# Kernel optimization log

Hardware: AMD Instinct MI355X
Metric: run time of the kernel (lower is better)

Reference implementation:

```python
import jax, jax.numpy as jnp
import numpy as np
import math

IN_CH = 512
KEY_SIZE = 512
VALUE_SIZE = 512
B, T = 8, 2048


def setup_inputs() -> dict:
    key = jax.random.key(0)
    ks = jax.random.split(key, 7)
    s = 1.0 / math.sqrt(IN_CH)
    return {
        "x": jax.random.normal(ks[0], (B, T, IN_CH), dtype=jnp.float32),
        "Wq": jax.random.uniform(ks[1], (IN_CH, KEY_SIZE), jnp.float32, -s, s),
        "bq": jax.random.uniform(ks[2], (KEY_SIZE,), jnp.float32, -s, s),
        "Wk": jax.random.uniform(ks[3], (IN_CH, KEY_SIZE), jnp.float32, -s, s),
        "bk": jax.random.uniform(ks[4], (KEY_SIZE,), jnp.float32, -s, s),
        "Wv": jax.random.uniform(ks[5], (IN_CH, VALUE_SIZE), jnp.float32, -s, s),
        "bv": jax.random.uniform(ks[6], (VALUE_SIZE,), jnp.float32, -s, s),
    }


def reference(x, Wq, bq, Wk, bk, Wv, bv):
    # Projections (single head)
    q = jnp.einsum('btc,ck->btk', x, Wq) + bq  # [B,T,K]
    k = jnp.einsum('btc,ck->btk', x, Wk) + bk  # [B,T,K]
    v = jnp.einsum('btc,cv->btv', x, Wv) + bv  # [B,T,V]
    # Full score matrix, causal mask (strictly upper triangle masked: col > row)
    scores = jnp.einsum('bqk,btk->bqt', q, k)  # [B,T,T]
    t = scores.shape[1]
    causal = jnp.arange(t)[None, :] > jnp.arange(t)[:, None]  # True where future
    scores = jnp.where(causal[None], -jnp.inf, scores)
    attn = jax.nn.softmax(scores / math.sqrt(KEY_SIZE), axis=2)
    out = jnp.einsum('bqt,btv->bqv', attn, v)  # [B,T,V]
    return jnp.concatenate((x, out), axis=2)  # [B,T,C+V]
```

## Files before the change

### kernel.cpp

```cpp
#include <hip/hip_runtime.h>


#define DEV __device__ __forceinline__

typedef unsigned short u16;
typedef unsigned int u32;
typedef __attribute__((ext_vector_type(8))) short short8;
typedef __attribute__((ext_vector_type(4))) float float4v;

DEV u16 f2bf(float f) {
    u32 u = __float_as_uint(f);
    return (u16)((u + 0x7FFFu + ((u >> 16) & 1u)) >> 16);
}
DEV float bf2f(u16 h) { return __uint_as_float(((u32)h) << 16); }

DEV float4v mfma16(short8 a, short8 b, float4v c) {
    return __builtin_amdgcn_mfma_f32_16x16x32_bf16(a, b, c, 0, 0, 0);
}

#define GLD16(gptr, lptr)                                                     \
    __builtin_amdgcn_global_load_lds(                                         \
        (const __attribute__((address_space(1))) void*)(gptr),                \
        (__attribute__((address_space(3))) void*)(lptr), 16, 0, 0)

__global__ void detect_k(const u32* __restrict__ xw, int* __restrict__ flag) {
    __shared__ int sh[256];
    int tid = threadIdx.x;
    u32 w = xw[tid * 64];
    int e = (w >> 7) & 0xFF;
    sh[tid] = (e >= 0x60 && e <= 0x90) ? 1 : 0;
    __syncthreads();
    for (int s = 128; s > 0; s >>= 1) {
        if (tid < s) sh[tid] += sh[tid + s];
        __syncthreads();
    }
    if (tid == 0) flag[0] = (sh[0] > 128) ? 1 : 0;
}

__global__ void convx_k(const void* __restrict__ x, const int* __restrict__ flag,
                        u16* __restrict__ xb, void* __restrict__ out) {
    int i0 = (blockIdx.x * 256 + threadIdx.x) * 8;
    int row = i0 >> 9, col = i0 & 511;
    if (flag[0]) {
        uint4 v = *(const uint4*)((const u16*)x + i0);
        *(uint4*)&xb[i0] = v;
        *(uint4*)((u16*)out + (size_t)row * 1024 + col) = v;
    } else {
        const float* xf = (const float*)x;
        float4 f0 = *(const float4*)(xf + i0);
        float4 f1 = *(const float4*)(xf + i0 + 4);
        union { u16 us[8]; uint4 v; } pk;
        pk.us[0] = f2bf(f0.x); pk.us[1] = f2bf(f0.y);
        pk.us[2] = f2bf(f0.z); pk.us[3] = f2bf(f0.w);
        pk.us[4] = f2bf(f1.x); pk.us[5] = f2bf(f1.y);
        pk.us[6] = f2bf(f1.z); pk.us[7] = f2bf(f1.w);
        *(uint4*)&xb[i0] = pk.v;
        float* o = (float*)out + (size_t)row * 1024 + col;
        *(float4*)o = f0; *(float4*)(o + 4) = f1;
    }
}

__global__ void convwb_k(const void* __restrict__ Wq, const void* __restrict__ Wk,
                         const void* __restrict__ Wv, const void* __restrict__ bq,
                         const void* __restrict__ bk, const void* __restrict__ bv,
                         const int* __restrict__ flag,
                         u16* __restrict__ Wt, u16* __restrict__ bbuf) {
    int z = blockIdx.y;
    if (blockIdx.x >= 1024) {
        int i = (blockIdx.x - 1024) * 256 + threadIdx.x;
        const void* s = (z == 0) ? bq : ((z == 1) ? bk : bv);
        bbuf[z * 512 + i] = flag[0] ? ((const u16*)s)[i]
                                    : f2bf(((const float*)s)[i]);
        return;
    }
    const void* W = (z == 0) ? Wq : ((z == 1) ? Wk : Wv);
    int flat = blockIdx.x * 256 + threadIdx.x;
    int n = flat >> 9, k = flat & 511;
    u16 v = flag[0] ? ((const u16*)W)[k * 512 + n]
                    : f2bf(((const float*)W)[k * 512 + n]);
    Wt[z * 262144 + flat] = v;
}

__global__ __launch_bounds__(256) void proj_k(
        const u16* __restrict__ x, const u16* __restrict__ Wt,
        const u16* __restrict__ bb,
        u16* __restrict__ Qo, u16* __restrict__ Ko, u16* __restrict__ Vt_out) {
    int z = blockIdx.z;
    const u16* Wz = Wt + z * 262144;
    const u16* bias = bb + z * 512;
    int mBase = blockIdx.x * 128;
    int nBase = blockIdx.y * 128;

    __shared__ __attribute__((aligned(16))) u16 Xs[128 * 32];
    __shared__ __attribute__((aligned(16))) u16 Ws[128 * 32];

    int tid = threadIdx.x;
    int w = tid >> 6, lane = tid & 63, quad = lane >> 4, l16 = lane & 15;
    int wr = (w >> 1) * 64, wc = (w & 1) * 64;

    float4v acc[4][4] = {};

    for (int k0 = 0; k0 < 512; k0 += 32) {
        #pragma unroll
        for (int gg = 0; gg < 2; gg++) {
            int g = w * 2 + gg;
            int row = g * 16 + (lane >> 2);
            int col8 = lane & 3;
            GLD16(&x [(size_t)(mBase + row) * 512 + k0 + col8 * 8], &Xs[g * 512]);
            GLD16(&Wz[(size_t)(nBase + row) * 512 + k0 + col8 * 8], &Ws[g * 512]);
        }
        __syncthreads();

        short8 a[4], b[4];
        #pragma unroll
        for (int mt = 0; mt < 4; mt++)
            a[mt] = *(const short8*)&Xs[(wr + mt * 16 + l16) * 32 + quad * 8];
        #pragma unroll
        for (int nt = 0; nt < 4; nt++)
            b[nt] = *(const short8*)&Ws[(wc + nt * 16 + l16) * 32 + quad * 8];
        #pragma unroll
        for (int mt = 0; mt < 4; mt++)
            #pragma unroll
            for (int nt = 0; nt < 4; nt++)
                acc[mt][nt] = mfma16(a[mt], b[nt], acc[mt][nt]);
        __syncthreads();
    }

    #pragma unroll
    for (int nt = 0; nt < 4; nt++) {
        int n = nBase + wc + nt * 16 + l16;
        float bval = bf2f(bias[n]);
        #pragma unroll
        for (int mt = 0; mt < 4; mt++) {
            int m0 = mBase + wr + mt * 16 + quad * 4;
            float4v v = acc[mt][nt];
            if (z == 2) {
                int bbi = m0 >> 11, tt = m0 & 2047;
                u16 t0 = f2bf(v[0] + bval), t1 = f2bf(v[1] + bval);
                u16 t2 = f2bf(v[2] + bval), t3 = f2bf(v[3] + bval);
                uint2 pk = make_uint2((u32)t0 | ((u32)t1 << 16), (u32)t2 | ((u32)t3 << 16));
                *(uint2*)&Vt_out[((size_t)bbi * 512 + n) * 2048 + tt] = pk;
            } else {
                u16* dst = (z == 0) ? Qo : Ko;
                #pragma unroll
                for (int r = 0; r < 4; r++)
                    dst[(size_t)(m0 + r) * 512 + n] = f2bf(v[r] + bval);
            }
        }
    }
}


#define LOADK(dst, kB, half)                                                  \
    { _Pragma("unroll")                                                       \
      for (int j = 0; j < 8; j++) {                                           \
        int row2 = 2 * (j * 4 + w);                                           \
        int row = row2 + (lane >> 5);                                         \
        int col8 = lane & 31;                                                 \
        GLD16(&Kb[(size_t)((kB) + row) * 512 + (half) * 256 +                 \
                  ((col8 ^ (row & 7)) << 3)], &dst[row2 * 256]);              \
      } }

#define LOADV(dst, kB, half)                                                  \
    { _Pragma("unroll")                                                       \
      for (int j = 0; j < 8; j++) {                                           \
        int blk8 = 8 * (j * 4 + w);                                           \
        int dl = blk8 + (lane >> 3);                                          \
        int col8 = lane & 7;                                                  \
        GLD16(&Vb[(size_t)((half) * 256 + dl) * 2048 + (kB) +                 \
                  ((col8 ^ (dl & 7)) << 3)], &dst[blk8 * 64]);                \
      } }

#define SSTEP(buf, h)                                                         \
    { _Pragma("unroll")                                                       \
      for (int kk = 0; kk < 8; kk++) {                                        \
        _Pragma("unroll")                                                     \
        for (int nt = 0; nt < 4; nt++) {                                      \
          short8 bf = *(const short8*)&buf[(nt * 16 + l16) * 256 +            \
                                           (((kk * 4 + quad) ^ sw) << 3)];    \
          accS[nt] = mfma16(qf[(h) * 8 + kk], bf, accS[nt]);                  \
        } } }

#define PVSTEP(buf, accO)                                                     \
    { _Pragma("unroll")                                                       \
      for (int kk = 0; kk < 2; kk++) {                                        \
        _Pragma("unroll")                                                     \
        for (int dt = 0; dt < 4; dt++) {                                      \
          int rowv = w * 64 + dt * 16 + l16;                                  \
          short8 bf = *(const short8*)&buf[rowv * 64 +                        \
                                           (((kk * 4 + quad) ^ sw) << 3)];    \
          _Pragma("unroll")                                                   \
          for (int mt = 0; mt < 4; mt++)                                      \
            accO[dt][mt] = mfma16(pf[mt][kk], bf, accO[dt][mt]);              \
        } } }

__global__ __launch_bounds__(256, 1) void attn_k(
        const u16* __restrict__ Q, const u16* __restrict__ K,
        const u16* __restrict__ Vt, const int* __restrict__ flag,
        void* __restrict__ out, u16* __restrict__ Opart,
        float2* __restrict__ ml, int dosplit) {
    int blk = blockIdx.x;
    int b, qt, h, kt0, kt1;
    if (dosplit) {
        qt = (blk < 256) ? (31 - (blk >> 4)) : ((blk - 256) >> 4);
        h  = (blk >> 3) & 1;
        b  = blk & 7;
        int n = qt + 1, mid = n >> 1;
        kt0 = h ? mid : 0;
        kt1 = h ? n : mid;
    } else {
        qt = 31 - (blk >> 3);
        h  = 0;
        b  = blk & 7;
        kt0 = 0; kt1 = qt + 1;
    }
    int q0 = qt * 64;
    int isbf = flag[0];

    __shared__ __attribute__((aligned(16))) u16 KV0[16384];
    __shared__ __attribute__((aligned(16))) u16 KV1[16384];
    __shared__ __attribute__((aligned(16))) u16 Ps[4096];
    __shared__ float al_s[64];
    __shared__ float il_s[64];

    int tid = threadIdx.x;
    int w = tid >> 6, lane = tid & 63, quad = lane >> 4, l16 = lane & 15;
    int sw = l16 & 7;

    const u16* Qb = Q  + (size_t)b * 2048 * 512;
    const u16* Kb = K  + (size_t)b * 2048 * 512;
    const u16* Vb = Vt + (size_t)b * 512 * 2048;

    if (kt0 < kt1) LOADK(KV0, kt0 * 64, 0);

    short8 qf[16];
    {
        const u16* Qrow = &Qb[(size_t)(q0 + w * 16 + l16) * 512];
        #pragma unroll
        for (int g = 0; g < 16; g++)
            qf[g] = *(const short8*)&Qrow[g * 32 + quad * 8];
    }

    float4v accO0[4][4] = {};
    float4v accO1[4][4] = {};
    float4v accS[4] = {};
    short8 pf[4][2];
    float mrow[4] = {-1e30f, -1e30f, -1e30f, -1e30f};
    float lrow[4] = {0.f, 0.f, 0.f, 0.f};
    const float scale = 0.044194173824159216f;

    __syncthreads();

    for (int kt = kt0; kt < kt1; kt++) {
        int kB = kt * 64;

        LOADK(KV1, kB, 1);
        SSTEP(KV0, 0);
        __syncthreads();

        LOADV(KV0, kB, 0);
        SSTEP(KV1, 1);
        {
            int diag = (kt == qt);
            float pv[4][4], alpha[4];
            #pragma unroll
            for (int r = 0; r < 4; r++) {
                float mx = -1e30f;
                #pragma unroll
                for (int nt = 0; nt < 4; nt++) {
                    float sv = accS[nt][r] * scale;
                    if (diag && (nt * 16 + l16 > w * 16 + quad * 4 + r)) sv = -1e30f;
                    pv[nt][r] = sv;
                    mx = fmaxf(mx, sv);
                }
                mx = fmaxf(mx, __shfl_xor(mx, 1));
                mx = fmaxf(mx, __shfl_xor(mx, 2));
                mx = fmaxf(mx, __shfl_xor(mx, 4));
                mx = fmaxf(mx, __shfl_xor(mx, 8));
                float mnew = fmaxf(mrow[r], mx);
                float a = __expf(mrow[r] - mnew);
                float sum = 0.f;
                #pragma unroll
                for (int nt = 0; nt < 4; nt++) {
                    pv[nt][r] = __expf(pv[nt][r] - mnew);
                    sum += pv[nt][r];
                }
                sum += __shfl_xor(sum, 1);
                sum += __shfl_xor(sum, 2);
                sum += __shfl_xor(sum, 4);
                sum += __shfl_xor(sum, 8);
                lrow[r] = lrow[r] * a + sum;
                mrow[r] = mnew;
                alpha[r] = a;
            }
            #pragma unroll
            for (int nt = 0; nt < 4; nt++)
                #pragma unroll
                for (int r = 0; r < 4; r++)
                    Ps[(w * 16 + quad * 4 + r) * 64 + nt * 16 + l16] = f2bf(pv[nt][r]);
            #pragma unroll
            for (int r = 0; r < 4; r++) al_s[w * 16 + quad * 4 + r] = alpha[r];
            #pragma unroll
            for (int nt = 0; nt < 4; nt++) accS[nt] = (float4v){0.f, 0.f, 0.f, 0.f};
        }
        __syncthreads();

        LOADV(KV1, kB, 1);
        {
            #pragma unroll
            for (int mt = 0; mt < 4; mt++)
                #pragma unroll
                for (int kk = 0; kk < 2; kk++)
                    pf[mt][kk] = *(const short8*)&Ps[(mt * 16 + l16) * 64 +
                                                     kk * 32 + quad * 8];
            float alf[4][4];
            #pragma unroll
            for (int mt = 0; mt < 4; mt++)
                #pragma unroll
                for (int r = 0; r < 4; r++)
                    alf[mt][r] = al_s[mt * 16 + quad * 4 + r];
            #pragma unroll
            for (int dt = 0; dt < 4; dt++)
                #pragma unroll
                for (int mt = 0; mt < 4; mt++)
                    #pragma unroll
                    for (int r = 0; r < 4; r++) {
                        accO0[dt][mt][r] *= alf[mt][r];
                        accO1[dt][mt][r] *= alf[mt][r];
                    }
        }
        PVSTEP(KV0, accO0);
        __syncthreads();

        if (kt + 1 < kt1) LOADK(KV0, kB + 64, 0);
        PVSTEP(KV1, accO1);
        __syncthreads();
    }

    if (dosplit) {
        if (l16 == 0) {
            #pragma unroll
            for (int r = 0; r < 4; r++) {
                int grow = b * 2048 + q0 + w * 16 + quad * 4 + r;
                ml[h * 16384 + grow] = make_float2(mrow[r], lrow[r]);
            }
        }
        #pragma unroll
        for (int dt = 0; dt < 4; dt++) {
            int dg = w * 64 + dt * 16 + l16;
            #pragma unroll
            for (int mt = 0; mt < 4; mt++)
                #pragma unroll
                for (int r = 0; r < 4; r++) {
                    int grow = b * 2048 + q0 + mt * 16 + quad * 4 + r;
                    size_t base = ((size_t)h * 16384 + grow) * 512;
                    Opart[base + dg]       = f2bf(accO0[dt][mt][r]);
                    Opart[base + dg + 256] = f2bf(accO1[dt][mt][r]);
                }
        }
    } else {
        #pragma unroll
        for (int r = 0; r < 4; r++) il_s[w * 16 + quad * 4 + r] = 1.0f / lrow[r];
        __syncthreads();
        float invl[4][4];
        #pragma unroll
        for (int mt = 0; mt < 4; mt++)
            #pragma unroll
            for (int r = 0; r < 4; r++) invl[mt][r] = il_s[mt * 16 + quad * 4 + r];
        u16*   o16 = (u16*)out;
        float* o32 = (float*)out;
        #pragma unroll
        for (int dt = 0; dt < 4; dt++) {
            int dg0 = 512 + w * 64 + dt * 16 + l16;
            #pragma unroll
            for (int mt = 0; mt < 4; mt++)
                #pragma unroll
                for (int r = 0; r < 4; r++) {
                    int rowg = q0 + mt * 16 + quad * 4 + r;
                    size_t base = ((size_t)b * 2048 + rowg) * 1024;
                    float v0 = accO0[dt][mt][r] * invl[mt][r];
                    float v1 = accO1[dt][mt][r] * invl[mt][r];
                    if (isbf) {
                        o16[base + dg0]       = f2bf(v0);
                        o16[base + dg0 + 256] = f2bf(v1);
                    } else {
                        o32[base + dg0]       = v0;
                        o32[base + dg0 + 256] = v1;
                    }
                }
        }
    }
}

__global__ __launch_bounds__(256) void combine_k(
        const u16* __restrict__ Opart, const float2* __restrict__ ml,
        const int* __restrict__ flag, void* __restrict__ out) {
    int tid = threadIdx.x;
    int grow = blockIdx.x * 4 + (tid >> 6);
    int d0 = (tid & 63) * 8;
    float2 ml0 = ml[grow], ml1 = ml[16384 + grow];
    float m = fmaxf(ml0.x, ml1.x);
    float a0 = __expf(ml0.x - m), a1 = __expf(ml1.x - m);
    float il = 1.0f / (ml0.y * a0 + ml1.y * a1);
    a0 *= il; a1 *= il;
    uint4 v0 = *(const uint4*)&Opart[(size_t)grow * 512 + d0];
    uint4 v1 = *(const uint4*)&Opart[(size_t)(16384 + grow) * 512 + d0];
    const u16* u0 = (const u16*)&v0;
    const u16* u1 = (const u16*)&v1;
    float res[8];
    #pragma unroll
    for (int i = 0; i < 8; i++)
        res[i] = bf2f(u0[i]) * a0 + bf2f(u1[i]) * a1;
    size_t base = (size_t)grow * 1024 + 512 + d0;
    if (flag[0]) {
        union { u16 us[8]; uint4 v; } pk;
        #pragma unroll
        for (int i = 0; i < 8; i++) pk.us[i] = f2bf(res[i]);
        *(uint4*)((u16*)out + base) = pk.v;
    } else {
        float* o = (float*)out + base;
        *(float4*)o = make_float4(res[0], res[1], res[2], res[3]);
        *(float4*)(o + 4) = make_float4(res[4], res[5], res[6], res[7]);
    }
}

extern "C" void kernel_launch(void* const* d_in, const int* in_sizes, int n_in,
                              void* d_out, int out_size, void* d_ws, size_t ws_size,
                              hipStream_t stream) {
    const void* x  = d_in[0];
    const void* Wq = d_in[1];
    const void* bq = d_in[2];
    const void* Wk = d_in[3];
    const void* bk = d_in[4];
    const void* Wv = d_in[5];
    const void* bv = d_in[6];

    u16* base = (u16*)d_ws;
    int* flag = (int*)base;
    u16* Wt   = base + 8;
    u16* bb   = Wt + 786432;
    u16* xb   = bb + 1544;
    u16* Qw   = xb + 8388608;
    u16* Kw   = Qw + 8388608;
    u16* Vtw  = Kw + 8388608;
    u16* Opart = Vtw + 8388608;
    float2* mlb = (float2*)(Opart + 16777216);

    size_t need = ((size_t)(Opart - base) + 16777216) * 2 + 262144;
    int dosplit = (ws_size >= need) ? 1 : 0;

    hipLaunchKernelGGL(detect_k, dim3(1), dim3(256), 0, stream, (const u32*)x, flag);
    hipLaunchKernelGGL(convx_k, dim3(4096), dim3(256), 0, stream, x, flag, xb, d_out);
    hipLaunchKernelGGL(convwb_k, dim3(1026, 3), dim3(256), 0, stream,
                       Wq, Wk, Wv, bq, bk, bv, flag, Wt, bb);
    hipLaunchKernelGGL(proj_k, dim3(128, 4, 3), dim3(256), 0, stream, xb, Wt, bb, Qw, Kw, Vtw);
    if (dosplit) {
        hipLaunchKernelGGL(attn_k, dim3(512), dim3(256), 0, stream,
                           Qw, Kw, Vtw, flag, d_out, Opart, mlb, 1);
        hipLaunchKernelGGL(combine_k, dim3(4096), dim3(256), 0, stream,
                           Opart, mlb, flag, d_out);
    } else {
        hipLaunchKernelGGL(attn_k, dim3(256), dim3(256), 0, stream,
                           Qw, Kw, Vtw, flag, d_out, Opart, mlb, 0);
    }
}
```

Before: 289.7 us.

## Quarter-chunk K/V staging with four LDS buffers and fine-grained vmcnt barriers

Splits each K and V tile into four 128-column chunks held in four 16KB LDS buffers instead of two 32KB halves. The loads are pipelined so that three chunks stay in flight, using explicit s_waitcnt vmcnt barriers in place of __syncthreads. MFMA sections are wrapped in s_setprio, and launch bounds are raised to allow two blocks per CU. The aim is better overlap of global-to-LDS loads with MFMA work and higher occupancy. The risks are register pressure from the launch bound change and correctness depending on the hand-counted vmcnt values.

```diff
diff --git a/kernel.cpp b/kernel.cpp
--- a/kernel.cpp
+++ b/kernel.cpp
@@ -151,50 +151,61 @@
 }
 
 
-#define LOADK(dst, kB, half)                                                  \
+#define LOADK_C(dst, kB, c)                                                   \
     { _Pragma("unroll")                                                       \
-      for (int j = 0; j < 8; j++) {                                           \
-        int row2 = 2 * (j * 4 + w);                                           \
-        int row = row2 + (lane >> 5);                                         \
-        int col8 = lane & 31;                                                 \
-        GLD16(&Kb[(size_t)((kB) + row) * 512 + (half) * 256 +                 \
-                  ((col8 ^ (row & 7)) << 3)], &dst[row2 * 256]);              \
+      for (int j = 0; j < 4; j++) {                                           \
+        int r4 = 4 * (j * 4 + w);                                             \
+        int row = r4 + (lane >> 4);                                           \
+        int g = lane & 15;                                                    \
+        GLD16(&Kb[(size_t)((kB) + row) * 512 + (c) * 128 +                    \
+                  ((g ^ (row & 7)) << 3)], &(dst)[r4 * 128]);                 \
       } }
 
-#define LOADV(dst, kB, half)                                                  \
+#define LOADV_C(dst, kB, c)                                                   \
     { _Pragma("unroll")                                                       \
-      for (int j = 0; j < 8; j++) {                                           \
-        int blk8 = 8 * (j * 4 + w);                                           \
-        int dl = blk8 + (lane >> 3);                                          \
-        int col8 = lane & 7;                                                  \
-        GLD16(&Vb[(size_t)((half) * 256 + dl) * 2048 + (kB) +                 \
-                  ((col8 ^ (dl & 7)) << 3)], &dst[blk8 * 64]);                \
+      for (int j = 0; j < 4; j++) {                                           \
+        int r8 = 8 * (j * 4 + w);                                             \
+        int dl = r8 + (lane >> 3);                                            \
+        int g = lane & 7;                                                     \
+        GLD16(&Vb[(size_t)((c) * 128 + dl) * 2048 + (kB) +                    \
+                  ((g ^ (dl & 7)) << 3)], &(dst)[r8 * 64]);                   \
       } }
 
-#define SSTEP(buf, h)                                                         \
-    { _Pragma("unroll")                                                       \
-      for (int kk = 0; kk < 8; kk++) {                                        \
+#define SSTEP_C(buf, c)                                                       \
+    { __builtin_amdgcn_s_setprio(1);                                          \
+      _Pragma("unroll")                                                       \
+      for (int kk = 0; kk < 4; kk++) {                                        \
         _Pragma("unroll")                                                     \
         for (int nt = 0; nt < 4; nt++) {                                      \
-          short8 bf = *(const short8*)&buf[(nt * 16 + l16) * 256 +            \
-                                           (((kk * 4 + quad) ^ sw) << 3)];    \
-          accS[nt] = mfma16(qf[(h) * 8 + kk], bf, accS[nt]);                  \
-        } } }
-
-#define PVSTEP(buf, accO)                                                     \
-    { _Pragma("unroll")                                                       \
+          short8 bf = *(const short8*)&(buf)[(nt * 16 + l16) * 128 +          \
+                                             (((kk * 4 + quad) ^ sw) << 3)];  \
+          accS[nt] = mfma16(qf[(c) * 4 + kk], bf, accS[nt]);                  \
+        } }                                                                   \
+      __builtin_amdgcn_s_setprio(0); }
+
+#define PVSTEP_C(buf, c)                                                      \
+    { __builtin_amdgcn_s_setprio(1);                                          \
+      _Pragma("unroll")                                                       \
       for (int kk = 0; kk < 2; kk++) {                                        \
         _Pragma("unroll")                                                     \
-        for (int dt = 0; dt < 4; dt++) {                                      \
-          int rowv = w * 64 + dt * 16 + l16;                                  \
-          short8 bf = *(const short8*)&buf[rowv * 64 +                        \
-                                           (((kk * 4 + quad) ^ sw) << 3)];    \
+        for (int dt = 0; dt < 2; dt++) {                                      \
+          int rowv = w * 32 + dt * 16 + l16;                                  \
+          short8 bf = *(const short8*)&(buf)[rowv * 64 +                      \
+                                             (((kk * 4 + quad) ^ sw) << 3)];  \
           _Pragma("unroll")                                                   \
           for (int mt = 0; mt < 4; mt++)                                      \
-            accO[dt][mt] = mfma16(pf[mt][kk], bf, accO[dt][mt]);              \
-        } } }
-
-__global__ __launch_bounds__(256, 1) void attn_k(
+            accO[(c)][dt][mt] = mfma16(pf[mt][kk], bf, accO[(c)][dt][mt]);    \
+        } }                                                                   \
+      __builtin_amdgcn_s_setprio(0); }
+
+#define WB(N)                                                                 \
+    do {                                                                      \
+        asm volatile("s_waitcnt vmcnt(" #N ") lgkmcnt(0)" ::: "memory");      \
+        __builtin_amdgcn_s_barrier();                                         \
+        asm volatile("" ::: "memory");                                        \
+    } while (0)
+
+__global__ __launch_bounds__(256, 2) void attn_k(
         const u16* __restrict__ Q, const u16* __restrict__ K,
         const u16* __restrict__ Vt, const int* __restrict__ flag,
         void* __restrict__ out, u16* __restrict__ Opart,
@@ -217,8 +228,7 @@
     int q0 = qt * 64;
     int isbf = flag[0];
 
-    __shared__ __attribute__((aligned(16))) u16 KV0[16384];
-    __shared__ __attribute__((aligned(16))) u16 KV1[16384];
+    __shared__ __attribute__((aligned(16))) u16 KV[4][8192];
     __shared__ __attribute__((aligned(16))) u16 Ps[4096];
     __shared__ float al_s[64];
     __shared__ float il_s[64];
@@ -231,8 +241,6 @@
     const u16* Kb = K  + (size_t)b * 2048 * 512;
     const u16* Vb = Vt + (size_t)b * 512 * 2048;
 
-    if (kt0 < kt1) LOADK(KV0, kt0 * 64, 0);
-
     short8 qf[16];
     {
         const u16* Qrow = &Qb[(size_t)(q0 + w * 16 + l16) * 512];
@@ -240,26 +248,39 @@
         for (int g = 0; g < 16; g++)
             qf[g] = *(const short8*)&Qrow[g * 32 + quad * 8];
     }
-
-    float4v accO0[4][4] = {};
-    float4v accO1[4][4] = {};
+    __builtin_amdgcn_sched_barrier(0);
+
+    if (kt0 < kt1) {
+        int kB0 = kt0 * 64;
+        LOADK_C(KV[0], kB0, 0);
+        LOADK_C(KV[1], kB0, 1);
+        LOADK_C(KV[2], kB0, 2);
+    }
+
+    float4v accO[4][2][4] = {};
     float4v accS[4] = {};
     short8 pf[4][2];
     float mrow[4] = {-1e30f, -1e30f, -1e30f, -1e30f};
     float lrow[4] = {0.f, 0.f, 0.f, 0.f};
     const float scale = 0.044194173824159216f;
 
-    __syncthreads();
-
     for (int kt = kt0; kt < kt1; kt++) {
         int kB = kt * 64;
-
-        LOADK(KV1, kB, 1);
-        SSTEP(KV0, 0);
-        __syncthreads();
-
-        LOADV(KV0, kB, 0);
-        SSTEP(KV1, 1);
+        int kBn = kB + 64;
+        int more = (kt + 1 < kt1);
+
+        WB(8);
+        LOADK_C(KV[3], kB, 3);
+        SSTEP_C(KV[0], 0);
+        WB(8);
+        LOADV_C(KV[0], kB, 0);
+        SSTEP_C(KV[1], 1);
+        WB(8);
+        LOADV_C(KV[1], kB, 1);
+        SSTEP_C(KV[2], 2);
+        WB(8);
+        LOADV_C(KV[2], kB, 2);
+        SSTEP_C(KV[3], 3);
         {
             int diag = (kt == qt);
             float pv[4][4], alpha[4];
@@ -303,9 +324,8 @@
             #pragma unroll
             for (int nt = 0; nt < 4; nt++) accS[nt] = (float4v){0.f, 0.f, 0.f, 0.f};
         }
-        __syncthreads();
-
-        LOADV(KV1, kB, 1);
+        WB(8);
+        LOADV_C(KV[3], kB, 3);
         {
             #pragma unroll
             for (int mt = 0; mt < 4; mt++)
@@ -320,21 +340,25 @@
                 for (int r = 0; r < 4; r++)
                     alf[mt][r] = al_s[mt * 16 + quad * 4 + r];
             #pragma unroll
-            for (int dt = 0; dt < 4; dt++)
-                #pragma unroll
-                for (int mt = 0; mt < 4; mt++)
+            for (int c = 0; c < 4; c++)
+                #pragma unroll
+                for (int dt = 0; dt < 2; dt++)
                     #pragma unroll
-                    for (int r = 0; r < 4; r++) {
-                        accO0[dt][mt][r] *= alf[mt][r];
-                        accO1[dt][mt][r] *= alf[mt][r];
-                    }
+                    for (int mt = 0; mt < 4; mt++)
+                        #pragma unroll
+                        for (int r = 0; r < 4; r++)
+                            accO[c][dt][mt][r] *= alf[mt][r];
         }
-        PVSTEP(KV0, accO0);
-        __syncthreads();
-
-        if (kt + 1 < kt1) LOADK(KV0, kB + 64, 0);
-        PVSTEP(KV1, accO1);
-        __syncthreads();
+        PVSTEP_C(KV[0], 0);
+        WB(8);
+        if (more) LOADK_C(KV[0], kBn, 0);
+        PVSTEP_C(KV[1], 1);
+        if (more) { WB(8); LOADK_C(KV[1], kBn, 1); }
+        else      { WB(4); }
+        PVSTEP_C(KV[2], 2);
+        if (more) { WB(8); LOADK_C(KV[2], kBn, 2); }
+        else      { WB(0); }
+        PVSTEP_C(KV[3], 3);
     }
 
     if (dosplit) {
@@ -346,18 +370,19 @@
             }
         }
         #pragma unroll
-        for (int dt = 0; dt < 4; dt++) {
-            int dg = w * 64 + dt * 16 + l16;
-            #pragma unroll
-            for (int mt = 0; mt < 4; mt++)
-                #pragma unroll
-                for (int r = 0; r < 4; r++) {
-                    int grow = b * 2048 + q0 + mt * 16 + quad * 4 + r;
-                    size_t base = ((size_t)h * 16384 + grow) * 512;
-                    Opart[base + dg]       = f2bf(accO0[dt][mt][r]);
-                    Opart[base + dg + 256] = f2bf(accO1[dt][mt][r]);
-                }
-        }
+        for (int c = 0; c < 4; c++)
+            #pragma unroll
+            for (int dt = 0; dt < 2; dt++) {
+                int dg = c * 128 + w * 32 + dt * 16 + l16;
+                #pragma unroll
+                for (int mt = 0; mt < 4; mt++)
+                    #pragma unroll
+                    for (int r = 0; r < 4; r++) {
+                        int grow = b * 2048 + q0 + mt * 16 + quad * 4 + r;
+                        Opart[((size_t)h * 16384 + grow) * 512 + dg] =
+                            f2bf(accO[c][dt][mt][r]);
+                    }
+            }
     } else {
         #pragma unroll
         for (int r = 0; r < 4; r++) il_s[w * 16 + quad * 4 + r] = 1.0f / lrow[r];
@@ -370,25 +395,21 @@
         u16*   o16 = (u16*)out;
         float* o32 = (float*)out;
         #pragma unroll
-        for (int dt = 0; dt < 4; dt++) {
-            int dg0 = 512 + w * 64 + dt * 16 + l16;
-            #pragma unroll
-            for (int mt = 0; mt < 4; mt++)
-                #pragma unroll
-                for (int r = 0; r < 4; r++) {
-                    int rowg = q0 + mt * 16 + quad * 4 + r;
-                    size_t base = ((size_t)b * 2048 + rowg) * 1024;
-                    float v0 = accO0[dt][mt][r] * invl[mt][r];
-                    float v1 = accO1[dt][mt][r] * invl[mt][r];
-                    if (isbf) {
-                        o16[base + dg0]       = f2bf(v0);
-                        o16[base + dg0 + 256] = f2bf(v1);
-                    } else {
-                        o32[base + dg0]       = v0;
-                        o32[base + dg0 + 256] = v1;
+        for (int c = 0; c < 4; c++)
+            #pragma unroll
+            for (int dt = 0; dt < 2; dt++) {
+                int dg0 = 512 + c * 128 + w * 32 + dt * 16 + l16;
+                #pragma unroll
+                for (int mt = 0; mt < 4; mt++)
+                    #pragma unroll
+                    for (int r = 0; r < 4; r++) {
+                        int rowg = q0 + mt * 16 + quad * 4 + r;
+                        size_t base = ((size_t)b * 2048 + rowg) * 1024;
+                        float v = accO[c][dt][mt][r] * invl[mt][r];
+                        if (isbf) o16[base + dg0] = f2bf(v);
+                        else      o32[base + dg0] = v;
                     }
-                }
-        }
+            }
     }
 }
 
```

Result: slower. 532.9 us (+84.0%).

## Double-buffer projection GEMM with swizzled LDS and lazy softmax rescale in attention

Applied to the files above, without the earlier changes.

The projection kernel now uses two LDS buffers with prefetch two steps ahead, explicit vmcnt waits and raw barriers, plus an XOR swizzle on the LDS columns to reduce bank conflicts. The attention kernel skips the running-max update and the rescale of the output accumulator when every row's new max is within a threshold of the old one, decided per wave and then per block through shared flags. This aims to overlap global loads with MFMA work and to remove redundant exp and scaling work. The cost is more complex synchronisation and a threshold-based skip that lets exponentials grow up to e^8 before renormalising.

```diff
diff --git a/kernel.cpp b/kernel.cpp
--- a/kernel.cpp
+++ b/kernel.cpp
@@ -81,6 +81,13 @@
     Wt[z * 262144 + flat] = v;
 }
 
+#define PWB(N)                                                                \
+    do {                                                                      \
+        asm volatile("s_waitcnt vmcnt(" #N ")" ::: "memory");                 \
+        __builtin_amdgcn_s_barrier();                                         \
+        asm volatile("" ::: "memory");                                        \
+    } while (0)
+
 __global__ __launch_bounds__(256) void proj_k(
         const u16* __restrict__ x, const u16* __restrict__ Wt,
         const u16* __restrict__ bb,
@@ -91,39 +98,56 @@
     int mBase = blockIdx.x * 128;
     int nBase = blockIdx.y * 128;
 
-    __shared__ __attribute__((aligned(16))) u16 Xs[128 * 32];
-    __shared__ __attribute__((aligned(16))) u16 Ws[128 * 32];
+    __shared__ __attribute__((aligned(16))) u16 Xs[2][128 * 32];
+    __shared__ __attribute__((aligned(16))) u16 Ws[2][128 * 32];
 
     int tid = threadIdx.x;
     int w = tid >> 6, lane = tid & 63, quad = lane >> 4, l16 = lane & 15;
     int wr = (w >> 1) * 64, wc = (w & 1) * 64;
 
+#define PISSUE(bi, k0)                                                        \
+    { _Pragma("unroll")                                                       \
+      for (int gg = 0; gg < 2; gg++) {                                        \
+        int g = w * 2 + gg;                                                   \
+        int row = g * 16 + (lane >> 2);                                       \
+        int c8 = (lane & 3) ^ ((row >> 1) & 3);                               \
+        GLD16(&x [(size_t)(mBase + row) * 512 + (k0) + c8 * 8], &Xs[bi][g * 512]); \
+        GLD16(&Wz[(size_t)(nBase + row) * 512 + (k0) + c8 * 8], &Ws[bi][g * 512]); \
+      } }
+
+    PISSUE(0, 0)
+    PISSUE(1, 32)
+
     float4v acc[4][4] = {};
 
-    for (int k0 = 0; k0 < 512; k0 += 32) {
-        #pragma unroll
-        for (int gg = 0; gg < 2; gg++) {
-            int g = w * 2 + gg;
-            int row = g * 16 + (lane >> 2);
-            int col8 = lane & 3;
-            GLD16(&x [(size_t)(mBase + row) * 512 + k0 + col8 * 8], &Xs[g * 512]);
-            GLD16(&Wz[(size_t)(nBase + row) * 512 + k0 + col8 * 8], &Ws[g * 512]);
-        }
-        __syncthreads();
+    #pragma unroll 2
+    for (int t = 0; t < 16; t++) {
+        int bi = t & 1;
+        if (t < 15) { PWB(4); } else { PWB(0); }
 
         short8 a[4], b[4];
         #pragma unroll
-        for (int mt = 0; mt < 4; mt++)
-            a[mt] = *(const short8*)&Xs[(wr + mt * 16 + l16) * 32 + quad * 8];
-        #pragma unroll
-        for (int nt = 0; nt < 4; nt++)
-            b[nt] = *(const short8*)&Ws[(wc + nt * 16 + l16) * 32 + quad * 8];
+        for (int mt = 0; mt < 4; mt++) {
+            int rr = wr + mt * 16 + l16;
+            a[mt] = *(const short8*)&Xs[bi][rr * 32 + ((quad ^ ((rr >> 1) & 3)) * 8)];
+        }
+        #pragma unroll
+        for (int nt = 0; nt < 4; nt++) {
+            int rr = wc + nt * 16 + l16;
+            b[nt] = *(const short8*)&Ws[bi][rr * 32 + ((quad ^ ((rr >> 1) & 3)) * 8)];
+        }
         #pragma unroll
         for (int mt = 0; mt < 4; mt++)
             #pragma unroll
             for (int nt = 0; nt < 4; nt++)
                 acc[mt][nt] = mfma16(a[mt], b[nt], acc[mt][nt]);
-        __syncthreads();
+
+        if (t < 14) {
+            asm volatile("s_waitcnt lgkmcnt(0)" ::: "memory");
+            __builtin_amdgcn_s_barrier();
+            asm volatile("" ::: "memory");
+            PISSUE(bi, (t + 2) * 32)
+        }
     }
 
     #pragma unroll
@@ -222,6 +246,7 @@
     __shared__ __attribute__((aligned(16))) u16 Ps[4096];
     __shared__ float al_s[64];
     __shared__ float il_s[64];
+    __shared__ int skip_s[4];
 
     int tid = threadIdx.x;
     int w = tid >> 6, lane = tid & 63, quad = lane >> 4, l16 = lane & 15;
@@ -262,7 +287,7 @@
         SSTEP(KV1, 1);
         {
             int diag = (kt == qt);
-            float pv[4][4], alpha[4];
+            float pv[4][4], mx4[4], alpha[4];
             #pragma unroll
             for (int r = 0; r < 4; r++) {
                 float mx = -1e30f;
@@ -277,8 +302,16 @@
                 mx = fmaxf(mx, __shfl_xor(mx, 2));
                 mx = fmaxf(mx, __shfl_xor(mx, 4));
                 mx = fmaxf(mx, __shfl_xor(mx, 8));
-                float mnew = fmaxf(mrow[r], mx);
-                float a = __expf(mrow[r] - mnew);
+                mx4[r] = mx;
+            }
+            int small = (mx4[0] - mrow[0] <= 8.f) && (mx4[1] - mrow[1] <= 8.f) &&
+                        (mx4[2] - mrow[2] <= 8.f) && (mx4[3] - mrow[3] <= 8.f);
+            int wskip = __all(small) ? 1 : 0;
+            if (lane == 0) skip_s[w] = wskip;
+            #pragma unroll
+            for (int r = 0; r < 4; r++) {
+                float mnew = wskip ? mrow[r] : fmaxf(mrow[r], mx4[r]);
+                float a = wskip ? 1.0f : __expf(mrow[r] - mnew);
                 float sum = 0.f;
                 #pragma unroll
                 for (int nt = 0; nt < 4; nt++) {
@@ -313,21 +346,24 @@
                 for (int kk = 0; kk < 2; kk++)
                     pf[mt][kk] = *(const short8*)&Ps[(mt * 16 + l16) * 64 +
                                                      kk * 32 + quad * 8];
-            float alf[4][4];
-            #pragma unroll
-            for (int mt = 0; mt < 4; mt++)
-                #pragma unroll
-                for (int r = 0; r < 4; r++)
-                    alf[mt][r] = al_s[mt * 16 + quad * 4 + r];
-            #pragma unroll
-            for (int dt = 0; dt < 4; dt++)
+            int bskip = skip_s[0] & skip_s[1] & skip_s[2] & skip_s[3];
+            if (!bskip) {
+                float alf[4][4];
                 #pragma unroll
                 for (int mt = 0; mt < 4; mt++)
                     #pragma unroll
-                    for (int r = 0; r < 4; r++) {
-                        accO0[dt][mt][r] *= alf[mt][r];
-                        accO1[dt][mt][r] *= alf[mt][r];
-                    }
+                    for (int r = 0; r < 4; r++)
+                        alf[mt][r] = al_s[mt * 16 + quad * 4 + r];
+                #pragma unroll
+                for (int dt = 0; dt < 4; dt++)
+                    #pragma unroll
+                    for (int mt = 0; mt < 4; mt++)
+                        #pragma unroll
+                        for (int r = 0; r < 4; r++) {
+                            accO0[dt][mt][r] *= alf[mt][r];
+                            accO1[dt][mt][r] *= alf[mt][r];
+                        }
+            }
         }
         PVSTEP(KV0, accO0);
         __syncthreads();
```

Measured after the change: 286.0 us. About the same (-1.2%).
